# Kernel tuning notes

Measured on AMD Instinct MI355X. Metric: run time of the kernel, lower is better.

The kernel has to match this reference:

```python
import jax, jax.numpy as jnp
import numpy as np

DIM = 768

def setup_inputs() -> dict:
    key = jax.random.key(0)
    ks = jax.random.split(key, 11)
    B, N = 4, 2048
    s = 1.0 / np.sqrt(DIM)
    inp = {
        "q": jax.random.normal(ks[0], (B, N, DIM), jnp.float32),
        "k": jax.random.normal(ks[1], (B, N, DIM), jnp.float32),
        "v": jax.random.normal(ks[2], (B, N, DIM), jnp.float32),
        "Wq": jax.random.normal(ks[3], (DIM, DIM), jnp.float32) * s,
        "bq": jnp.zeros((DIM,), jnp.float32),
        "Wk": jax.random.normal(ks[4], (DIM, DIM), jnp.float32) * s,
        "bk": jnp.zeros((DIM,), jnp.float32),
        "Wv": jax.random.normal(ks[5], (DIM, DIM), jnp.float32) * s,
        "bv": jnp.zeros((DIM,), jnp.float32),
        "Wp": jax.random.normal(ks[6], (DIM, DIM), jnp.float32) * s,
        "bp": jnp.zeros((DIM,), jnp.float32),
    }
    return inp

def reference(q, k, v, Wq, bq, Wk, bk, Wv, bv, Wp, bp):
    # Linear projections (torch Linear: x @ W.T + b)
    scale = DIM ** (-0.5)  # note: full dim, num_heads unused in original forward
    qp = q @ Wq.T + bq            # [B, Nq, D]
    kp = k @ Wk.T + bk            # [B, Nk, D]
    vp = v @ Wv.T + bv            # [B, Nk, D]
    attn = jnp.einsum('bqd,bkd->bqk', qp * scale, kp)  # [B, Nq, Nk]
    attn = jax.nn.softmax(attn, axis=-1)
    x = jnp.einsum('bqk,bkd->bqd', attn, vp)           # [B, Nq, D]
    return x @ Wp.T + bp
```

## Files before the change

kernel.cpp:

```cpp
#include <hip/hip_runtime.h>
#include <hip/hip_bf16.h>
#include <math.h>

typedef __bf16 bf16x8 __attribute__((ext_vector_type(8)));
typedef float  f32x4  __attribute__((ext_vector_type(4)));
typedef float  f32x4v __attribute__((ext_vector_type(4)));
typedef unsigned short ushort_t;
typedef ushort_t u16x4 __attribute__((ext_vector_type(4)));
typedef ushort_t u16x8 __attribute__((ext_vector_type(8)));

__device__ __forceinline__ ushort_t f2bf(float f) {
    unsigned u = __builtin_bit_cast(unsigned, f);
    u += 0x7FFFu + ((u >> 16) & 1u);
    return (ushort_t)(u >> 16);
}
__device__ __forceinline__ float bf2f(ushort_t b) {
    return __builtin_bit_cast(float, (unsigned)b << 16);
}

__device__ __forceinline__ void xcd_remap(int& bx, int& by, int& bz) {
    const int gx = gridDim.x, gy = gridDim.y;
    const int nwg = gx * gy * gridDim.z;
    const int lin = (blockIdx.z * gy + blockIdx.y) * gx + blockIdx.x;
    const int chunk = nwg >> 3;
    int nid = (lin & 7) * chunk + (lin >> 3);
    bx = nid % gx; nid /= gx;
    by = nid % gy; bz = nid / gy;
}

__global__ __launch_bounds__(256) void cvt_multi(const float* __restrict__ i0, const float* __restrict__ i1,
                                                 const float* __restrict__ i2, const float* __restrict__ i3,
                                                 ushort_t* __restrict__ o0, ushort_t* __restrict__ o1,
                                                 ushort_t* __restrict__ o2, ushort_t* __restrict__ o3, int n4) {
    const int z = blockIdx.z;
    const float* in  = z == 0 ? i0 : z == 1 ? i1 : z == 2 ? i2 : i3;
    ushort_t*    out = z == 0 ? o0 : z == 1 ? o1 : z == 2 ? o2 : o3;
    int i = blockIdx.x * 256 + threadIdx.x;
    if (i >= n4) return;
    f32x4v v = ((const f32x4v*)in)[i];
    u16x4 o = { f2bf(v.x), f2bf(v.y), f2bf(v.z), f2bf(v.w) };
    ((u16x4*)out)[i] = o;
}

__global__ __launch_bounds__(256) void zero_f32(float* __restrict__ p, int n) {
    int i = blockIdx.x * 256 + threadIdx.x;
    if (i < n) p[i] = 0.f;
}

#define S_BARR asm volatile("s_barrier" ::: "memory")

#define PHASE8(tt_, q_, RDB_, STC_, STKT_, STARR_, STH_, VMW_)                              \
    { bf16x8 af[2][2];                                                                      \
      if (RDB_) rd_B((tt_), bfr);                                                           \
      rd_Aq((tt_), (q_), af);                                                               \
      if (STC_) stage_h((STKT_), (STARR_), (STH_));                                         \
      S_BARR;                                                                               \
      asm volatile("s_waitcnt lgkmcnt(0)" ::: "memory");                                    \
      __builtin_amdgcn_sched_barrier(0);                                                    \
      __builtin_amdgcn_s_setprio(1);                                                        \
      _Pragma("unroll") for (int m2 = 0; m2 < 2; ++m2)                                      \
      _Pragma("unroll") for (int ni = 0; ni < 4; ++ni)                                      \
      _Pragma("unroll") for (int kk = 0; kk < 2; ++kk)                                      \
          acc[(q_)*2 + m2][ni] = __builtin_amdgcn_mfma_f32_16x16x32_bf16(                   \
              af[m2][kk], bfr[ni][kk], acc[(q_)*2 + m2][ni], 0, 0, 0);                      \
      __builtin_amdgcn_s_setprio(0);                                                        \
      VMW_;                                                                                 \
      S_BARR; }

#define GEMM256_8PH(Ab_, lda_, Bb_, ldb_, Kdim_)                                            \
    __shared__ __align__(16) ushort_t lds[2][2][2][128 * 64];                               \
    const int tid  = threadIdx.x;                                                           \
    const int lane = tid & 63;                                                              \
    const int wave = tid >> 6;                                                              \
    const int wm = wave >> 2, wn = wave & 3;                                                \
    const int r16 = lane & 15, kb = lane >> 4;                                              \
    f32x4 acc[8][4];                                                                        \
    _Pragma("unroll") for (int i_ = 0; i_ < 8; ++i_)                                        \
        _Pragma("unroll") for (int j_ = 0; j_ < 4; ++j_)                                    \
            acc[i_][j_] = (f32x4){0.f, 0.f, 0.f, 0.f};                                      \
    auto stage_h = [&](int kt, int arr, int h) {                                            \
        const int d  = kt & 1;                                                              \
        const int k0 = kt * 64;                                                             \
        _Pragma("unroll") for (int l = 0; l < 2; ++l) {                                     \
            const int idx = l * 512 + tid;                                                  \
            const int row = idx >> 3, sl = idx & 7;                                         \
            const int ssrc = sl ^ (row & 7);                                                \
            const long long grow = h * 128 + row;                                           \
            const ushort_t* g = (arr == 0)                                                  \
                ? (Ab_) + (tM + grow) * (long long)(lda_) + k0 + ssrc * 8                   \
                : (Bb_) + (tN + grow) * (long long)(ldb_) + k0 + ssrc * 8;                  \
            __builtin_amdgcn_global_load_lds((const __attribute__((address_space(1))) void*)g, \
                (__attribute__((address_space(3))) void*)&lds[d][arr][h][idx * 8], 16, 0, 0); \
        } };                                                                                \
    auto rd_B = [&](int kt, bf16x8 (&bfr_)[4][2]) {                                         \
        const int d = kt & 1;                                                               \
        _Pragma("unroll") for (int ni = 0; ni < 4; ++ni)                                    \
        _Pragma("unroll") for (int kk = 0; kk < 2; ++kk) {                                  \
            const int row = (wn & 1) * 64 + ni * 16 + r16;                                  \
            const int o16 = row * 8 + ((kk * 4 + kb) ^ (row & 7));                          \
            bfr_[ni][kk] = *(const bf16x8*)((const char*)&lds[d][1][wn >> 1][0] + o16 * 16);\
        } };                                                                                \
    auto rd_Aq = [&](int kt, int q, bf16x8 (&af_)[2][2]) {                                  \
        const int d = kt & 1;                                                               \
        _Pragma("unroll") for (int m2 = 0; m2 < 2; ++m2)                                    \
        _Pragma("unroll") for (int kk = 0; kk < 2; ++kk) {                                  \
            const int row = (q * 2 + m2) * 16 + r16;                                        \
            const int o16 = row * 8 + ((kk * 4 + kb) ^ (row & 7));                          \
            af_[m2][kk] = *(const bf16x8*)((const char*)&lds[d][0][wm][0] + o16 * 16);      \
        } };                                                                                \
    const int NT = (Kdim_) / 64;                                                            \
                          \
    stage_h(0, 1, 0); stage_h(0, 1, 1);                                                     \
    stage_h(0, 0, 0); stage_h(0, 0, 1);                                                     \
    stage_h(1, 1, 0); stage_h(1, 1, 1);                                                     \
    asm volatile("s_waitcnt vmcnt(4)" ::: "memory");                                        \
    S_BARR;                                                                                 \
    _Pragma("unroll 1") for (int it = 0; it < NT / 2; ++it) {                               \
        const int t = 2 * it;                                                               \
        const bool more = (t + 2 < NT);                                                     \
        bf16x8 bfr[4][2];                                                                   \
        PHASE8(t,     0, true,  true, t + 1, 0, 0, )                                        \
        PHASE8(t,     1, false, true, t + 1, 0, 1, )                                        \
        PHASE8(t,     2, false, more, t + 2, 1, 0, )                                        \
        PHASE8(t,     3, false, more, t + 2, 1, 1,                                          \
               if (more) asm volatile("s_waitcnt vmcnt(4)" ::: "memory");                   \
               else      asm volatile("s_waitcnt vmcnt(0)" ::: "memory"))                   \
        PHASE8(t + 1, 0, true,  more, t + 2, 0, 0, )                                        \
        PHASE8(t + 1, 1, false, more, t + 2, 0, 1, )                                        \
        PHASE8(t + 1, 2, false, more, t + 3, 1, 0, )                                        \
        PHASE8(t + 1, 3, false, more, t + 3, 1, 1,                                          \
               if (more) asm volatile("s_waitcnt vmcnt(4)" ::: "memory"))                   \
    }                                                                                       \
    const int rquad = (lane >> 4) * 4;                                                      \
    const int cl    = lane & 15;

__global__ __launch_bounds__(512, 2)
void projqk8(const ushort_t* __restrict__ qin, const ushort_t* __restrict__ kin,
             const ushort_t* __restrict__ Wqb, const ushort_t* __restrict__ Wkb,
             const float* __restrict__ bqv, const float* __restrict__ bkv,
             ushort_t* __restrict__ dq, ushort_t* __restrict__ dk)
{
    int bx, by, bz;
    xcd_remap(bx, by, bz);
    const int z = bz;
    const long long tM = (long long)by * 256;
    const long long tN = (long long)bx * 256;
    const ushort_t* Ab = z ? kin : qin;
    const ushort_t* Bb = z ? Wkb : Wqb;
    const float* bias  = z ? bkv : bqv;
    ushort_t* dst      = z ? dk : dq;

    GEMM256_8PH(Ab, 768, Bb, 768, 768)

#pragma unroll
    for (int mi = 0; mi < 8; ++mi) {
        const long long r = tM + wm * 128 + mi * 16 + rquad;
#pragma unroll
        for (int ni = 0; ni < 4; ++ni) {
            f32x4 v = acc[mi][ni];
            const long long c = tN + wn * 64 + ni * 16 + cl;
            const float bc = bias[c];
#pragma unroll
            for (int j = 0; j < 4; ++j)
                dst[(r + j) * 768 + c] = f2bf(v[j] + bc);
        }
    }
}

__global__ __launch_bounds__(512, 2)
void sexp_pv8(const ushort_t* __restrict__ qp, const ushort_t* __restrict__ kp,
              const ushort_t* __restrict__ Wvb, const ushort_t* __restrict__ vin,
              const float* __restrict__ bvv,
              ushort_t* __restrict__ P, float* __restrict__ rowsum,
              ushort_t* __restrict__ dvT, float scale)
{
    int bx, by, bz;
    xcd_remap(bx, by, bz);
    const int wid = bx;
    const bool is_pv = wid >= 256;
    long long tM, tN;
    const ushort_t *Ab, *Bb;
    int z = 0;
    if (!is_pv) {
        z = wid >> 6;
        const int w2 = wid & 63;
        tM = (long long)(w2 >> 3) * 256;
        tN = (long long)(w2 & 7) * 256;
        Ab = qp + (long long)z * 1572864;
        Bb = kp + (long long)z * 1572864;
    } else {
        const int pv = wid - 256;
        tM = (long long)(pv >> 5) * 256;
        tN = (long long)(pv & 31) * 256;
        Ab = Wvb;
        Bb = vin;
    }

    GEMM256_8PH(Ab, 768, Bb, 768, 768)

    if (!is_pv) {
        ushort_t* out = P + (long long)z * 4194304;
#pragma unroll
        for (int mi = 0; mi < 8; ++mi) {
            const long long r = tM + wm * 128 + mi * 16 + rquad;
            float rs[4] = {0.f, 0.f, 0.f, 0.f};
#pragma unroll
            for (int ni = 0; ni < 4; ++ni) {
                f32x4 v = acc[mi][ni];
                const long long c = tN + wn * 64 + ni * 16 + cl;
#pragma unroll
                for (int j = 0; j < 4; ++j) {
                    float p = __expf(v[j] * scale);
                    ushort_t pb = f2bf(p);
                    out[(r + j) * 2048 + c] = pb;
                    rs[j] += bf2f(pb);
                }
            }
#pragma unroll
            for (int j = 0; j < 4; ++j) {
                float s = rs[j];
                s += __shfl_xor(s, 1, 64);
                s += __shfl_xor(s, 2, 64);
                s += __shfl_xor(s, 4, 64);
                s += __shfl_xor(s, 8, 64);
                if (cl == 0) atomicAdd(&rowsum[(long long)z * 2048 + r + j], s);
            }
        }
    } else {
#pragma unroll
        for (int mi = 0; mi < 8; ++mi) {
            const long long r = tM + wm * 128 + mi * 16 + rquad;
#pragma unroll
            for (int ni = 0; ni < 4; ++ni) {
                f32x4 v = acc[mi][ni];
                const long long c = tN + wn * 64 + ni * 16 + cl;
#pragma unroll
                for (int j = 0; j < 4; ++j)
                    dvT[(r + j) * 8192 + c] = f2bf(v[j] + bvv[r + j]);
            }
        }
    }
}

#define M_PVN  1
#define M_OUT  2

#define BM 128
#define BN 128
#define BK 32

#define GEMM_CORE(Ab_, lda_, Bb_, ldb_, Kdim_)                                              \
    __shared__ __align__(16) ushort_t lds[2][2][BM * BK];                                   \
    const int tid  = threadIdx.x;                                                           \
    const int lane = tid & 63;                                                              \
    const int wave = tid >> 6;                                                              \
    const int wr = wave >> 1, wc = wave & 1;                                                \
    f32x4 acc[4][4];                                                                        \
    _Pragma("unroll") for (int i = 0; i < 4; ++i)                                           \
        _Pragma("unroll") for (int j = 0; j < 4; ++j)                                       \
            acc[i][j] = (f32x4){0.f, 0.f, 0.f, 0.f};                                        \
    auto stage = [&](int buf, int kt) {                                                     \
        const int k0 = kt * BK;                                                             \
        _Pragma("unroll") for (int rnd = 0; rnd < 2; ++rnd) {                               \
            const int c    = tid + rnd * 256;                                               \
            const int row  = c >> 2;                                                        \
            const int slot = (c & 3) ^ (row & 3);                                           \
            const ushort_t* ga = (Ab_) + (tM + row) * (long long)(lda_) + k0 + slot * 8;    \
            const ushort_t* gb = (Bb_) + (tN + row) * (long long)(ldb_) + k0 + slot * 8;    \
            ushort_t* la = &lds[buf][0][(rnd * 256 + wave * 64) * 8];                       \
            ushort_t* lb = &lds[buf][1][(rnd * 256 + wave * 64) * 8];                       \
            __builtin_amdgcn_global_load_lds((const __attribute__((address_space(1))) void*)ga, \
                                             (__attribute__((address_space(3))) void*)la, 16, 0, 0); \
            __builtin_amdgcn_global_load_lds((const __attribute__((address_space(1))) void*)gb, \
                                             (__attribute__((address_space(3))) void*)lb, 16, 0, 0); \
        }                                                                                   \
    };                                                                                      \
    auto compute = [&](int buf) {                                                           \
        const int kb  = lane >> 4;                                                          \
        const int r16 = lane & 15;                                                          \
        bf16x8 af[4], bfr[4];                                                               \
        _Pragma("unroll") for (int mi = 0; mi < 4; ++mi) {                                  \
            const int row = wr * 64 + mi * 16 + r16;                                        \
            const int off = row * 64 + ((kb ^ (row & 3)) << 4);                             \
            af[mi] = *(const bf16x8*)((const char*)lds[buf][0] + off);                      \
        }                                                                                   \
        _Pragma("unroll") for (int ni = 0; ni < 4; ++ni) {                                  \
            const int row = wc * 64 + ni * 16 + r16;                                        \
            const int off = row * 64 + ((kb ^ (row & 3)) << 4);                             \
            bfr[ni] = *(const bf16x8*)((const char*)lds[buf][1] + off);                     \
        }                                                                                   \
        _Pragma("unroll") for (int mi = 0; mi < 4; ++mi)                                    \
            _Pragma("unroll") for (int ni = 0; ni < 4; ++ni)                                \
                acc[mi][ni] = __builtin_amdgcn_mfma_f32_16x16x32_bf16(af[mi], bfr[ni], acc[mi][ni], 0, 0, 0); \
    };                                                                                      \
    const int NT = (Kdim_) / BK;                                                            \
    stage(0, 0);                                                                            \
    __syncthreads();                                                                        \
    int cur = 0;                                                                            \
    for (int kt = 0; kt + 1 < NT; ++kt) {                                                   \
        stage(cur ^ 1, kt + 1);                                                             \
        compute(cur);                                                                       \
        __syncthreads();                                                                    \
        cur ^= 1;                                                                           \
    }                                                                                       \
    compute(cur);                                                                           \
    const int rquad = (lane >> 4) * 4;                                                      \
    const int cl    = lane & 15;

template<int MODE>
__global__ __launch_bounds__(256, 3)
void gemm_nt(const ushort_t* __restrict__ A, int lda, long long aBatch,
             const ushort_t* __restrict__ B, int ldb, long long bBatch,
             void* __restrict__ Cv, int ldc, long long cBatch,
             const float* __restrict__ bias, float* __restrict__ rowsum,
             int K)
{
    int bx, by, bz;
    xcd_remap(bx, by, bz);
    const long long tM = (long long)by * BM;
    const long long tN = (long long)bx * BN;
    const int z = bz;
    const ushort_t* Ab = A + (long long)z * aBatch;
    const ushort_t* Bb = B + (long long)z * bBatch;

    GEMM_CORE(Ab, lda, Bb, ldb, K)

#pragma unroll
    for (int mi = 0; mi < 4; ++mi) {
        const long long r = tM + wr * 64 + mi * 16 + rquad;
        if constexpr (MODE == M_PVN) {
            ushort_t* out = (ushort_t*)Cv + (long long)z * cBatch;
            float inv[4];
#pragma unroll
            for (int j = 0; j < 4; ++j)
                inv[j] = 1.0f / rowsum[(long long)z * 2048 + r + j];
#pragma unroll
            for (int ni = 0; ni < 4; ++ni) {
                f32x4 v = acc[mi][ni];
                const long long c = tN + wc * 64 + ni * 16 + cl;
#pragma unroll
                for (int j = 0; j < 4; ++j)
                    out[(r + j) * ldc + c] = f2bf(v[j] * inv[j]);
            }
        } else {
            float* out = (float*)Cv;
#pragma unroll
            for (int ni = 0; ni < 4; ++ni) {
                f32x4 v = acc[mi][ni];
                const long long c = tN + wc * 64 + ni * 16 + cl;
                const float bc = bias[c];
#pragma unroll
                for (int j = 0; j < 4; ++j)
                    out[(r + j) * ldc + c] = v[j] + bc;
            }
        }
    }
}

extern "C" void kernel_launch(void* const* d_in, const int* in_sizes, int n_in,
                              void* d_out, int out_size, void* d_ws, size_t ws_size,
                              hipStream_t stream) {
    (void)in_sizes; (void)n_in; (void)out_size; (void)ws_size;
    const float* q  = (const float*)d_in[0];
    const float* k  = (const float*)d_in[1];
    const float* v  = (const float*)d_in[2];
    const float* Wq = (const float*)d_in[3];
    const float* bq = (const float*)d_in[4];
    const float* Wk = (const float*)d_in[5];
    const float* bk = (const float*)d_in[6];
    const float* Wv = (const float*)d_in[7];
    const float* bv = (const float*)d_in[8];
    const float* Wp = (const float*)d_in[9];
    const float* bp = (const float*)d_in[10];
    float* out = (float*)d_out;

    char* ws = (char*)d_ws;
    ushort_t* vb  = (ushort_t*)(ws);
    ushort_t* qb  = (ushort_t*)(ws + 12582912LL);
    ushort_t* kb  = (ushort_t*)(ws + 25165824LL);
    ushort_t* P   = (ushort_t*)(ws + 12582912LL);
    ushort_t* Wqb = (ushort_t*)(ws + 46137344LL);
    ushort_t* Wkb = (ushort_t*)(ws + 47316992LL);
    ushort_t* Wvb = (ushort_t*)(ws + 48496640LL);
    ushort_t* Wpb = (ushort_t*)(ws + 49676288LL);
    ushort_t* qp  = (ushort_t*)(ws + 50855936LL);
    ushort_t* kp  = (ushort_t*)(ws + 63438848LL);
    ushort_t* vpT = (ushort_t*)(ws + 76021760LL);
    float* rowsum = (float*)(ws + 88604672LL);
    ushort_t* Ob  = qp;

    const float scale = 1.0f / sqrtf(768.0f);

    cvt_multi<<<dim3(6144, 1, 3), 256, 0, stream>>>(q, k, v, nullptr, qb, kb, vb, nullptr, 1572864);
    cvt_multi<<<dim3(576, 1, 4), 256, 0, stream>>>(Wq, Wk, Wv, Wp, Wqb, Wkb, Wvb, Wpb, 147456);

    projqk8<<<dim3(3, 32, 2), 512, 0, stream>>>(qb, kb, Wqb, Wkb, bq, bk, qp, kp);

    zero_f32<<<32, 256, 0, stream>>>(rowsum, 8192);

    sexp_pv8<<<dim3(352, 1, 1), 512, 0, stream>>>(qp, kp, Wvb, vb, bv, P, rowsum, vpT, scale);

    gemm_nt<M_PVN><<<dim3(6, 16, 4), 256, 0, stream>>>(P, 2048, 4194304, vpT, 8192, 2048,
                                                       Ob, 768, 1572864, nullptr, rowsum, 2048);

    gemm_nt<M_OUT><<<dim3(6, 64, 1), 256, 0, stream>>>(Ob, 768, 0, Wpb, 768, 0, out, 768, 0, bp, nullptr, 768);
}
```

Measured before the change: 168.3 us.

## Restructure launch schedule: overlap V projection with q/k conversion, unroll GEMM pipeline

The 256x256 GEMM main loop becomes fully unrolled over 12 K-tiles with four phases per tile, replacing the two-tiles-per-iteration eight-phase loop. The V projection moves out of the score kernel into a new kernel that also does the fp32-to-bf16 conversion of q and k in its spare blocks. The score/exp kernel is now a plain 8x8x4 grid. The aim is to overlap conversion with the V GEMM and balance the score kernel, at the cost of more code size and a changed launch order.

```diff
diff --git a/kernel.cpp b/kernel.cpp
--- a/kernel.cpp
+++ b/kernel.cpp
@@ -47,27 +47,19 @@
     if (i < n) p[i] = 0.f;
 }
 
-#define S_BARR asm volatile("s_barrier" ::: "memory")
-
-#define PHASE8(tt_, q_, RDB_, STC_, STKT_, STARR_, STH_, VMW_)                              \
-    { bf16x8 af[2][2];                                                                      \
-      if (RDB_) rd_B((tt_), bfr);                                                           \
-      rd_Aq((tt_), (q_), af);                                                               \
-      if (STC_) stage_h((STKT_), (STARR_), (STH_));                                         \
-      S_BARR;                                                                               \
-      asm volatile("s_waitcnt lgkmcnt(0)" ::: "memory");                                    \
-      __builtin_amdgcn_sched_barrier(0);                                                    \
-      __builtin_amdgcn_s_setprio(1);                                                        \
-      _Pragma("unroll") for (int m2 = 0; m2 < 2; ++m2)                                      \
-      _Pragma("unroll") for (int ni = 0; ni < 4; ++ni)                                      \
-      _Pragma("unroll") for (int kk = 0; kk < 2; ++kk)                                      \
-          acc[(q_)*2 + m2][ni] = __builtin_amdgcn_mfma_f32_16x16x32_bf16(                   \
-              af[m2][kk], bfr[ni][kk], acc[(q_)*2 + m2][ni], 0, 0, 0);                      \
-      __builtin_amdgcn_s_setprio(0);                                                        \
-      VMW_;                                                                                 \
-      S_BARR; }
-
-#define GEMM256_8PH(Ab_, lda_, Bb_, ldb_, Kdim_)                                            \
+#define S_BARR   asm volatile("s_barrier" ::: "memory")
+#define LGKM0_SB asm volatile("s_waitcnt lgkmcnt(0)" ::: "memory"); __builtin_amdgcn_sched_barrier(0)
+
+#define MFMA16(q_)                                                                          \
+    __builtin_amdgcn_s_setprio(1);                                                          \
+    _Pragma("unroll") for (int m2 = 0; m2 < 2; ++m2)                                        \
+    _Pragma("unroll") for (int ni = 0; ni < 4; ++ni)                                        \
+    _Pragma("unroll") for (int kk = 0; kk < 2; ++kk)                                        \
+        acc[(q_)*2 + m2][ni] = __builtin_amdgcn_mfma_f32_16x16x32_bf16(                     \
+            af[m2][kk], bfr[ni][kk], acc[(q_)*2 + m2][ni], 0, 0, 0);                        \
+    __builtin_amdgcn_s_setprio(0)
+
+#define GEMM256_4PH(Ab_, lda_, Bb_, ldb_, NTv)                                              \
     __shared__ __align__(16) ushort_t lds[2][2][2][128 * 64];                               \
     const int tid  = threadIdx.x;                                                           \
     const int lane = tid & 63;                                                              \
@@ -108,34 +100,39 @@
             const int o16 = row * 8 + ((kk * 4 + kb) ^ (row & 7));                          \
             af_[m2][kk] = *(const bf16x8*)((const char*)&lds[d][0][wm][0] + o16 * 16);      \
         } };                                                                                \
-    const int NT = (Kdim_) / 64;                                                            \
-                          \
+                      \
     stage_h(0, 1, 0); stage_h(0, 1, 1);                                                     \
     stage_h(0, 0, 0); stage_h(0, 0, 1);                                                     \
     stage_h(1, 1, 0); stage_h(1, 1, 1);                                                     \
     asm volatile("s_waitcnt vmcnt(4)" ::: "memory");                                        \
     S_BARR;                                                                                 \
-    _Pragma("unroll 1") for (int it = 0; it < NT / 2; ++it) {                               \
-        const int t = 2 * it;                                                               \
-        const bool more = (t + 2 < NT);                                                     \
+    _Pragma("unroll") for (int t = 0; t < (NTv); ++t) {                                     \
         bf16x8 bfr[4][2];                                                                   \
-        PHASE8(t,     0, true,  true, t + 1, 0, 0, )                                        \
-        PHASE8(t,     1, false, true, t + 1, 0, 1, )                                        \
-        PHASE8(t,     2, false, more, t + 2, 1, 0, )                                        \
-        PHASE8(t,     3, false, more, t + 2, 1, 1,                                          \
-               if (more) asm volatile("s_waitcnt vmcnt(4)" ::: "memory");                   \
-               else      asm volatile("s_waitcnt vmcnt(0)" ::: "memory"))                   \
-        PHASE8(t + 1, 0, true,  more, t + 2, 0, 0, )                                        \
-        PHASE8(t + 1, 1, false, more, t + 2, 0, 1, )                                        \
-        PHASE8(t + 1, 2, false, more, t + 3, 1, 0, )                                        \
-        PHASE8(t + 1, 3, false, more, t + 3, 1, 1,                                          \
-               if (more) asm volatile("s_waitcnt vmcnt(4)" ::: "memory"))                   \
+        { bf16x8 af[2][2];                                                                  \
+          rd_B(t, bfr); rd_Aq(t, 0, af);                                                    \
+          if (t + 1 < (NTv)) stage_h(t + 1, 0, 0);                                          \
+          S_BARR; LGKM0_SB; MFMA16(0); S_BARR; }                                            \
+        { bf16x8 af[2][2];                                                                  \
+          rd_Aq(t, 1, af);                                                                  \
+          if (t + 1 < (NTv)) stage_h(t + 1, 0, 1);                                          \
+          S_BARR; LGKM0_SB; MFMA16(1); S_BARR; }                                            \
+        { bf16x8 af[2][2];                                                                  \
+          rd_Aq(t, 2, af);                                                                  \
+          if (t + 2 < (NTv)) stage_h(t + 2, 1, 0);                                          \
+          S_BARR; LGKM0_SB; MFMA16(2); S_BARR; }                                            \
+        { bf16x8 af[2][2];                                                                  \
+          rd_Aq(t, 3, af);                                                                  \
+          if (t + 2 < (NTv)) stage_h(t + 2, 1, 1);                                          \
+          S_BARR; LGKM0_SB; MFMA16(3);                                                      \
+          if (t == (NTv) - 2)      { asm volatile("s_waitcnt vmcnt(0)" ::: "memory"); }     \
+          else if (t < (NTv) - 2)  { asm volatile("s_waitcnt vmcnt(4)" ::: "memory"); }     \
+          S_BARR; }                                                                         \
     }                                                                                       \
     const int rquad = (lane >> 4) * 4;                                                      \
     const int cl    = lane & 15;
 
 __global__ __launch_bounds__(512, 2)
-void projqk8(const ushort_t* __restrict__ qin, const ushort_t* __restrict__ kin,
+void projqk4(const ushort_t* __restrict__ qin, const ushort_t* __restrict__ kin,
              const ushort_t* __restrict__ Wqb, const ushort_t* __restrict__ Wkb,
              const float* __restrict__ bqv, const float* __restrict__ bkv,
              ushort_t* __restrict__ dq, ushort_t* __restrict__ dk)
@@ -150,7 +147,7 @@
     const float* bias  = z ? bkv : bqv;
     ushort_t* dst      = z ? dk : dq;
 
-    GEMM256_8PH(Ab, 768, Bb, 768, 768)
+    GEMM256_4PH(Ab, 768, Bb, 768, 12)
 
 #pragma unroll
     for (int mi = 0; mi < 8; ++mi) {
@@ -168,76 +165,85 @@
 }
 
 __global__ __launch_bounds__(512, 2)
-void sexp_pv8(const ushort_t* __restrict__ qp, const ushort_t* __restrict__ kp,
-              const ushort_t* __restrict__ Wvb, const ushort_t* __restrict__ vin,
-              const float* __restrict__ bvv,
-              ushort_t* __restrict__ P, float* __restrict__ rowsum,
-              ushort_t* __restrict__ dvT, float scale)
+void sexp4(const ushort_t* __restrict__ qp, const ushort_t* __restrict__ kp,
+           ushort_t* __restrict__ P, float* __restrict__ rowsum, float scale)
 {
     int bx, by, bz;
     xcd_remap(bx, by, bz);
-    const int wid = bx;
-    const bool is_pv = wid >= 256;
-    long long tM, tN;
-    const ushort_t *Ab, *Bb;
-    int z = 0;
-    if (!is_pv) {
-        z = wid >> 6;
-        const int w2 = wid & 63;
-        tM = (long long)(w2 >> 3) * 256;
-        tN = (long long)(w2 & 7) * 256;
-        Ab = qp + (long long)z * 1572864;
-        Bb = kp + (long long)z * 1572864;
-    } else {
-        const int pv = wid - 256;
-        tM = (long long)(pv >> 5) * 256;
-        tN = (long long)(pv & 31) * 256;
-        Ab = Wvb;
-        Bb = vin;
+    const long long tM = (long long)by * 256;
+    const long long tN = (long long)bx * 256;
+    const int z = bz;
+    const ushort_t* Ab = qp + (long long)z * 1572864;
+    const ushort_t* Bb = kp + (long long)z * 1572864;
+
+    GEMM256_4PH(Ab, 768, Bb, 768, 12)
+
+    ushort_t* out = P + (long long)z * 4194304;
+#pragma unroll
+    for (int mi = 0; mi < 8; ++mi) {
+        const long long r = tM + wm * 128 + mi * 16 + rquad;
+        float rs[4] = {0.f, 0.f, 0.f, 0.f};
+#pragma unroll
+        for (int ni = 0; ni < 4; ++ni) {
+            f32x4 v = acc[mi][ni];
+            const long long c = tN + wn * 64 + ni * 16 + cl;
+#pragma unroll
+            for (int j = 0; j < 4; ++j) {
+                float p = __expf(v[j] * scale);
+                ushort_t pb = f2bf(p);
+                out[(r + j) * 2048 + c] = pb;
+                rs[j] += bf2f(pb);
+            }
+        }
+#pragma unroll
+        for (int j = 0; j < 4; ++j) {
+            float s = rs[j];
+            s += __shfl_xor(s, 1, 64);
+            s += __shfl_xor(s, 2, 64);
+            s += __shfl_xor(s, 4, 64);
+            s += __shfl_xor(s, 8, 64);
+            if (cl == 0) atomicAdd(&rowsum[(long long)z * 2048 + r + j], s);
+        }
     }
-
-    GEMM256_8PH(Ab, 768, Bb, 768, 768)
-
-    if (!is_pv) {
-        ushort_t* out = P + (long long)z * 4194304;
+}
+
+__global__ __launch_bounds__(512, 2)
+void vprojcvt(const ushort_t* __restrict__ wv_, const ushort_t* __restrict__ vb_,
+              const float* __restrict__ bv_, ushort_t* __restrict__ dvT_,
+              const float* __restrict__ qf_, const float* __restrict__ kf_,
+              ushort_t* __restrict__ qb_, ushort_t* __restrict__ kb_)
+{
+    if (blockIdx.x < 96) {
+        const int id = blockIdx.x;
+        const long long tM = (long long)(id % 3) * 256;
+        const long long tN = (long long)(id / 3) * 256;
+        const ushort_t* Ab = wv_;
+        const ushort_t* Bb = vb_;
+
+        GEMM256_4PH(Ab, 768, Bb, 768, 12)
+
 #pragma unroll
         for (int mi = 0; mi < 8; ++mi) {
             const long long r = tM + wm * 128 + mi * 16 + rquad;
-            float rs[4] = {0.f, 0.f, 0.f, 0.f};
 #pragma unroll
             for (int ni = 0; ni < 4; ++ni) {
                 f32x4 v = acc[mi][ni];
                 const long long c = tN + wn * 64 + ni * 16 + cl;
 #pragma unroll
-                for (int j = 0; j < 4; ++j) {
-                    float p = __expf(v[j] * scale);
-                    ushort_t pb = f2bf(p);
-                    out[(r + j) * 2048 + c] = pb;
-                    rs[j] += bf2f(pb);
-                }
+                for (int j = 0; j < 4; ++j)
+                    dvT_[(r + j) * 8192 + c] = f2bf(v[j] + bv_[r + j]);
             }
-#pragma unroll
-            for (int j = 0; j < 4; ++j) {
-                float s = rs[j];
-                s += __shfl_xor(s, 1, 64);
-                s += __shfl_xor(s, 2, 64);
-                s += __shfl_xor(s, 4, 64);
-                s += __shfl_xor(s, 8, 64);
-                if (cl == 0) atomicAdd(&rowsum[(long long)z * 2048 + r + j], s);
-            }
         }
     } else {
-#pragma unroll
-        for (int mi = 0; mi < 8; ++mi) {
-            const long long r = tM + wm * 128 + mi * 16 + rquad;
-#pragma unroll
-            for (int ni = 0; ni < 4; ++ni) {
-                f32x4 v = acc[mi][ni];
-                const long long c = tN + wn * 64 + ni * 16 + cl;
-#pragma unroll
-                for (int j = 0; j < 4; ++j)
-                    dvT[(r + j) * 8192 + c] = f2bf(v[j] + bvv[r + j]);
-            }
+        const long long stride = 160LL * 512;
+        for (long long i = (long long)(blockIdx.x - 96) * 512 + threadIdx.x;
+             i < 2LL * 1572864; i += stride) {
+            const float* src; ushort_t* dst; long long off;
+            if (i < 1572864) { src = qf_; dst = qb_; off = i; }
+            else             { src = kf_; dst = kb_; off = i - 1572864; }
+            f32x4v v4 = ((const f32x4v*)src)[off];
+            u16x4 o = { f2bf(v4.x), f2bf(v4.y), f2bf(v4.z), f2bf(v4.w) };
+            ((u16x4*)dst)[off] = o;
         }
     }
 }
@@ -391,17 +397,18 @@
 
     const float scale = 1.0f / sqrtf(768.0f);
 
-    cvt_multi<<<dim3(6144, 1, 3), 256, 0, stream>>>(q, k, v, nullptr, qb, kb, vb, nullptr, 1572864);
+    cvt_multi<<<dim3(6144, 1, 1), 256, 0, stream>>>(v, nullptr, nullptr, nullptr,
+                                                    vb, nullptr, nullptr, nullptr, 1572864);
     cvt_multi<<<dim3(576, 1, 4), 256, 0, stream>>>(Wq, Wk, Wv, Wp, Wqb, Wkb, Wvb, Wpb, 147456);
-
-    projqk8<<<dim3(3, 32, 2), 512, 0, stream>>>(qb, kb, Wqb, Wkb, bq, bk, qp, kp);
-
     zero_f32<<<32, 256, 0, stream>>>(rowsum, 8192);
 
-    sexp_pv8<<<dim3(352, 1, 1), 512, 0, stream>>>(qp, kp, Wvb, vb, bv, P, rowsum, vpT, scale);
+    vprojcvt<<<256, 512, 0, stream>>>(Wvb, vb, bv, vpT, q, k, qb, kb);
+
+    projqk4<<<dim3(3, 32, 2), 512, 0, stream>>>(qb, kb, Wqb, Wkb, bq, bk, qp, kp);
+
+    sexp4<<<dim3(8, 8, 4), 512, 0, stream>>>(qp, kp, P, rowsum, scale);
 
     gemm_nt<M_PVN><<<dim3(6, 16, 4), 256, 0, stream>>>(P, 2048, 4194304, vpT, 8192, 2048,
                                                        Ob, 768, 1572864, nullptr, rowsum, 2048);
-
     gemm_nt<M_OUT><<<dim3(6, 64, 1), 256, 0, stream>>>(Ob, 768, 0, Wpb, 768, 0, out, 768, 0, bp, nullptr, 768);
 }
```

Result: no change. 167.6 us (-0.4%).
